# Kernel tuning notes

Measured on AMD Instinct MI355X. Metric: run time of the kernel, lower is better.

Reference implementation:

```python
import jax, jax.numpy as jnp
import numpy as np
from jax.ops import segment_sum

N_GRAPHS, N_PER = 100, 1000
N = N_GRAPHS * N_PER
DEG = 32
E = N * DEG
RATIO = 0.8
K = int(np.ceil(RATIO * N_PER))  # 800, equal-size graphs -> fixed k
F_IN, F_MID, F_OUT = 128, 16, 256


def setup_inputs() -> dict:
    key = jax.random.key(0)
    ks = jax.random.split(key, 10)
    x = jax.random.normal(ks[0], (N, F_IN), dtype=jnp.float32)
    # intra-graph random edges
    epg = E // N_GRAPHS
    src_l = jax.random.randint(ks[1], (N_GRAPHS, epg), 0, N_PER)
    dst_l = jax.random.randint(ks[2], (N_GRAPHS, epg), 0, N_PER)
    offs = (jnp.arange(N_GRAPHS) * N_PER)[:, None]
    edge_index = jnp.stack([(src_l + offs).reshape(-1), (dst_l + offs).reshape(-1)]).astype(jnp.int32)
    batch = jnp.repeat(jnp.arange(N_GRAPHS, dtype=jnp.int32), N_PER)
    s = lambda fan: 1.0 / np.sqrt(fan)
    W1 = jax.random.normal(ks[3], (F_IN, F_MID), dtype=jnp.float32) * s(F_IN)
    b1 = jnp.zeros((F_MID,), dtype=jnp.float32)
    w_rel = jax.random.normal(ks[4], (F_MID, 1), dtype=jnp.float32) * s(F_MID)
    b_rel = jnp.zeros((1,), dtype=jnp.float32)
    w_root = jax.random.normal(ks[5], (F_MID, 1), dtype=jnp.float32) * s(F_MID)
    W2 = jax.random.normal(ks[6], (F_MID, F_OUT), dtype=jnp.float32) * s(F_MID)
    b2 = jnp.zeros((F_OUT,), dtype=jnp.float32)
    return {"x": x, "edge_index": edge_index, "batch": batch,
            "W1": W1, "b1": b1, "w_rel": w_rel, "b_rel": b_rel,
            "w_root": w_root, "W2": W2, "b2": b2}


def _gcn(x, src, dst, W, b, self_w, ew, n):
    # GCNConv with self-loops: D^{-1/2}(A+I)D^{-1/2} X W + b; masked variant
    deg = segment_sum(ew, dst, num_segments=n) + self_w
    dis = jnp.where(deg > 0, jax.lax.rsqrt(deg), 0.0)
    xw = x @ W
    coef = ew * dis[src] * dis[dst]                       # [E]
    agg = segment_sum(xw[src] * coef[:, None], dst, num_segments=n)
    agg = agg + xw * (self_w * dis * dis)[:, None]        # self-loop term
    return agg + b


def reference(x, edge_index, batch, W1, b1, w_rel, b_rel, w_root, W2, b2):
    src, dst = edge_index[0], edge_index[1]
    ones_n = jnp.ones((N,), dtype=x.dtype)
    ones_e = jnp.ones((src.shape[0],), dtype=x.dtype)
    # conv1 + relu
    h = jax.nn.relu(_gcn(x, src, dst, W1, b1, ones_n, ones_e, N))
    # SAGPooling score: GraphConv(16,1) -> tanh
    agg = segment_sum(h[src], dst, num_segments=N)
    score = jnp.tanh((agg @ w_rel + h @ w_root + b_rel)[:, 0])  # [N]
    # per-graph top-k (equal graph sizes -> fixed K), expressed as node mask
    sc2 = score.reshape(N_GRAPHS, N_PER)
    _, idx = jax.lax.top_k(sc2, K)
    mask = jnp.zeros((N_GRAPHS, N_PER), dtype=x.dtype)
    mask = mask.at[jnp.arange(N_GRAPHS)[:, None], idx].set(1.0).reshape(-1)  # [N]
    h = h * (score * mask)[:, None]                       # x[perm] * score[perm]
    em = mask[src] * mask[dst]                            # filter_adj as edge mask
    # conv2 + relu on surviving nodes only
    h2 = jax.nn.relu(_gcn(h, src, dst, W2, b2, mask, em, N)) * mask[:, None]
    # global mean pool over surviving nodes per graph
    sums = segment_sum(h2, batch, num_segments=N_GRAPHS)
    cnt = segment_sum(mask, batch, num_segments=N_GRAPHS)
    return sums / cnt[:, None]
```

## Files before the change

kernel.cpp:

```cpp
#include <hip/hip_runtime.h>
#include <math.h>

#define N_NODES 100000
#define NG 100
#define N_PER 1000
#define N_EDGES 3200000
#define EPG 32000
#define EPG4 8000
#define EPGP 35008
#define K_TOP 800
#define F_IN 128
#define F_MID 16
#define F_OUT 256
#define SENT 1000
#define NCH 8
#define CHN 128

typedef __attribute__((ext_vector_type(8))) short short8;
typedef __attribute__((ext_vector_type(4))) float floatx4;

__device__ __forceinline__ unsigned short f2bf(float x) {
    union { float f; unsigned int u; } c; c.f = x;
    unsigned int u = c.u;
    u = u + 0x7FFF + ((u >> 16) & 1);
    return (unsigned short)(u >> 16);
}
__device__ __forceinline__ void add4(float4& a, const float4 b) {
    a.x += b.x; a.y += b.y; a.z += b.z; a.w += b.w;
}
__device__ __forceinline__ int fidx4(int s, int l) {
    return s * 16 + ((4 * (l + ((s >> 1) & 3))) & 15);
}
__device__ __forceinline__ unsigned int fkey(float f) {
    unsigned int u = __float_as_uint(f);
    return (u & 0x80000000u) ? ~u : (u | 0x80000000u);
}

__global__ __launch_bounds__(1024) void k_front(const float* __restrict__ x,
    const float* __restrict__ W1, const int* __restrict__ ei,
    unsigned short* __restrict__ csr, int* __restrict__ crG,
    float* __restrict__ dis1G, float* __restrict__ xw1)
{
    __shared__ int cnts[N_PER];
    __shared__ int rs[N_PER];
    __shared__ int wtot[64];
    __shared__ __align__(16) unsigned short csrl[EPGP];

    int b = blockIdx.x, t = threadIdx.x;
    if (b < NG) {
        int g = b, ebase = g * EPG, nbase = g * N_PER;
        if (b == 0 && t < F_MID) xw1[(size_t)N_NODES * F_MID + t] = 0.f;
        const int4* dst4 = (const int4*)(ei + N_EDGES + ebase);
        const int4* src4 = (const int4*)(ei + ebase);
        if (t < N_PER) cnts[t] = 0;
        __syncthreads();
        uint2 spk[8], dpk[8];
        unsigned rkreg[8];
#pragma unroll
        for (int j = 0; j < 8; j++) {
            int i = t + (j << 10);
            if (i < EPG4) {
                int4 s = src4[i];
                int4 d = dst4[i];
                unsigned dl0 = (unsigned)(d.x - nbase), dl1 = (unsigned)(d.y - nbase);
                unsigned dl2 = (unsigned)(d.z - nbase), dl3 = (unsigned)(d.w - nbase);
                spk[j].x = (unsigned)(s.x - nbase) | ((unsigned)(s.y - nbase) << 16);
                spk[j].y = (unsigned)(s.z - nbase) | ((unsigned)(s.w - nbase) << 16);
                dpk[j].x = dl0 | (dl1 << 16);
                dpk[j].y = dl2 | (dl3 << 16);
                unsigned r0 = (unsigned)atomicAdd(&cnts[dl0], 1);
                unsigned r1 = (unsigned)atomicAdd(&cnts[dl1], 1);
                unsigned r2 = (unsigned)atomicAdd(&cnts[dl2], 1);
                unsigned r3 = (unsigned)atomicAdd(&cnts[dl3], 1);
                rkreg[j] = r0 | (r1 << 8) | (r2 << 16) | (r3 << 24);
            }
        }
        __syncthreads();
        if (t < 64) {
            volatile int* vt = wtot;
            int base = t << 4;
            int lex[16]; int run = 0;
#pragma unroll
            for (int j = 0; j < 16; j++) {
                int idx = base + j;
                int c4j = (idx < N_PER) ? ((cnts[idx] + 3) & ~3) : 0;
                lex[j] = run; run += c4j;
            }
            vt[t] = run;
#pragma unroll
            for (int d = 1; d < 64; d <<= 1) {
                int v = (t >= d) ? vt[t - d] : 0;
                vt[t] = vt[t] + v;
            }
            int off = vt[t] - run;
#pragma unroll
            for (int j = 0; j < 16; j++) {
                int idx = base + j;
                if (idx < N_PER) rs[idx] = off + lex[j];
            }
        }
        __syncthreads();
        int c = (t < N_PER) ? cnts[t] : 0;
        int c4 = (c + 3) & ~3;
        if (t < N_PER) {
            int exc = rs[t];
            crG[nbase + t] = (c << 16) | exc;
            dis1G[nbase + t] = rsqrtf((float)c + 1.0f);
            for (int q = c; q < c4; q++) csrl[exc + q] = (unsigned short)SENT;
        }
        __syncthreads();
#pragma unroll
        for (int j = 0; j < 8; j++) {
            int i = t + (j << 10);
            if (i < EPG4) {
                unsigned rk = rkreg[j];
                unsigned dx = dpk[j].x, dy = dpk[j].y;
                unsigned sx = spk[j].x, sy = spk[j].y;
                csrl[rs[dx & 0xFFFFu] + (rk & 255u)]          = (unsigned short)(sx & 0xFFFFu);
                csrl[rs[dx >> 16]     + ((rk >> 8) & 255u)]   = (unsigned short)(sx >> 16);
                csrl[rs[dy & 0xFFFFu] + ((rk >> 16) & 255u)]  = (unsigned short)(sy & 0xFFFFu);
                csrl[rs[dy >> 16]     + (rk >> 24)]           = (unsigned short)(sy >> 16);
            }
        }
        __syncthreads();
        {
            const uint4* sv = (const uint4*)csrl;
            uint4* dv = (uint4*)(csr + (size_t)g * EPGP);
            for (int i = t; i < EPGP / 8; i += 1024) dv[i] = sv[i];
        }
    } else {
        int n = (b - NG) * 1024 + t;
        if (n >= N_NODES) return;
        const float4* xr = (const float4*)(x + (size_t)n * F_IN);
        float4 a0 = {0,0,0,0}, a1 = a0, a2 = a0, a3 = a0;
#pragma unroll 4
        for (int kk = 0; kk < 32; kk++) {
            float4 xv = xr[kk];
#pragma unroll
            for (int r = 0; r < 4; r++) {
                const float4* wr = (const float4*)(W1 + (kk * 4 + r) * F_MID);
                float xs = (r == 0) ? xv.x : (r == 1) ? xv.y : (r == 2) ? xv.z : xv.w;
                float4 w0 = wr[0], w1 = wr[1], w2 = wr[2], w3 = wr[3];
                a0.x = fmaf(xs, w0.x, a0.x); a0.y = fmaf(xs, w0.y, a0.y);
                a0.z = fmaf(xs, w0.z, a0.z); a0.w = fmaf(xs, w0.w, a0.w);
                a1.x = fmaf(xs, w1.x, a1.x); a1.y = fmaf(xs, w1.y, a1.y);
                a1.z = fmaf(xs, w1.z, a1.z); a1.w = fmaf(xs, w1.w, a1.w);
                a2.x = fmaf(xs, w2.x, a2.x); a2.y = fmaf(xs, w2.y, a2.y);
                a2.z = fmaf(xs, w2.z, a2.z); a2.w = fmaf(xs, w2.w, a2.w);
                a3.x = fmaf(xs, w3.x, a3.x); a3.y = fmaf(xs, w3.y, a3.y);
                a3.z = fmaf(xs, w3.z, a3.z); a3.w = fmaf(xs, w3.w, a3.w);
            }
        }
        float4* op = (float4*)(xw1 + (size_t)n * F_MID);
        op[0] = a0; op[1] = a1; op[2] = a2; op[3] = a3;
    }
}

__global__ __launch_bounds__(512) void k_conv1(const unsigned short* __restrict__ csr,
    const int* __restrict__ crG,
    const float* __restrict__ dis1G, const float* __restrict__ xw1,
    const float* __restrict__ b1, const float* __restrict__ w_rel,
    const float* __restrict__ w_root,
    float* __restrict__ hG, float* __restrict__ hwG, float* __restrict__ hroG)
{
    __shared__ __align__(16) float feat[(N_PER + 1) * F_MID];
    int t = threadIdx.x, b = blockIdx.x;
    int g = b % NG, chunk = b / NG;
    int nbase = g * N_PER;
    const unsigned short* cg = csr + (size_t)g * EPGP;
    {
        const float4* xsrc = (const float4*)(xw1 + (size_t)nbase * F_MID);
        for (int i = t; i < N_PER * 4; i += 512) {
            int nn = i >> 2, q = i & 3;
            float4 v = xsrc[i];
            float d = dis1G[nbase + nn];
            v.x *= d; v.y *= d; v.z *= d; v.w *= d;
            *(float4*)(feat + fidx4(nn, q)) = v;
        }
        if (t < 4) { float4 z = {0.f, 0.f, 0.f, 0.f}; *(float4*)(feat + fidx4(SENT, t)) = z; }
    }
    __syncthreads();

    int grp = t >> 2, l = t & 3;
    int n = chunk * CHN + grp;
    if (n >= N_PER) return;
    int cr = crG[nbase + n];
    int c4 = ((cr >> 16) + 3) & ~3;
    const unsigned short* cp = cg + (cr & 0xFFFF);
    float4 a0 = {0,0,0,0}, a1 = a0, a2 = a0, a3 = a0;
    for (int k = 0; k < c4; k += 4) {
        uint2 wv = *(const uint2*)(cp + k);
        int s0 = wv.x & 0xFFFF, s1 = wv.x >> 16, s2 = wv.y & 0xFFFF, s3 = wv.y >> 16;
        add4(a0, *(const float4*)(feat + fidx4(s0, l)));
        add4(a1, *(const float4*)(feat + fidx4(s1, l)));
        add4(a2, *(const float4*)(feat + fidx4(s2, l)));
        add4(a3, *(const float4*)(feat + fidx4(s3, l)));
    }
    add4(a0, a1); add4(a2, a3); add4(a0, a2);
    float dn = dis1G[nbase + n];
    float4 sf = *(const float4*)(feat + fidx4(n, l));
    float4 b14 = *(const float4*)(b1 + 4 * l);
    float4 hv;
    hv.x = fmaxf(fmaf(dn, a0.x + sf.x, b14.x), 0.f);
    hv.y = fmaxf(fmaf(dn, a0.y + sf.y, b14.y), 0.f);
    hv.z = fmaxf(fmaf(dn, a0.z + sf.z, b14.z), 0.f);
    hv.w = fmaxf(fmaf(dn, a0.w + sf.w, b14.w), 0.f);
    *(float4*)(hG + ((size_t)(nbase + n) << 4) + 4 * l) = hv;

    float4 wr4 = *(const float4*)(w_rel + 4 * l);
    float4 wo4 = *(const float4*)(w_root + 4 * l);
    float p1 = hv.x * wr4.x + hv.y * wr4.y + hv.z * wr4.z + hv.w * wr4.w;
    float p2 = hv.x * wo4.x + hv.y * wo4.y + hv.z * wo4.z + hv.w * wo4.w;
    p1 += __shfl_xor(p1, 1); p1 += __shfl_xor(p1, 2);
    p2 += __shfl_xor(p2, 1); p2 += __shfl_xor(p2, 2);
    if (l == 0) { hwG[nbase + n] = p1; hroG[nbase + n] = p2; }
}

__global__ __launch_bounds__(1024) void k_mid(const unsigned short* __restrict__ csr,
    const int* __restrict__ crG,
    const float* __restrict__ hwG, const float* __restrict__ hroG,
    const float* __restrict__ b_rel,
    float* __restrict__ mskG, float* __restrict__ dis2G, float* __restrict__ wsrcG,
    float* __restrict__ out)
{
    __shared__ float hwl[N_PER + 1];
    __shared__ float sc[N_PER];
    __shared__ float msk[N_PER + 1];
    __shared__ int cntl[N_PER];
    __shared__ int rsl[N_PER];
    __shared__ int hist[1024];
    __shared__ int wtot[64];
    __shared__ int sh_b1, sh_r1, sh_b2, sh_r2, sh_len, sh_cntgt, sh_T;
    __shared__ float sh_thr;

    int t = threadIdx.x, g = blockIdx.x;
    int nbase = g * N_PER;
    const unsigned short* cg = csr + (size_t)g * EPGP;
    int grp = t >> 2, l = t & 3;

    if (t < N_PER) {
        int cr = crG[nbase + t];
        cntl[t] = cr >> 16; rsl[t] = cr & 0xFFFF;
        hwl[t] = hwG[nbase + t];
    }
    if (t == 0) { sh_cntgt = 0; sh_len = 0; hwl[SENT] = 0.f; }
    if (t < F_OUT) out[g * F_OUT + t] = 0.f;
    float brel = b_rel[0];
    __syncthreads();

#pragma unroll
    for (int rr = 0; rr < 4; rr++) {
        int n = grp + 256 * rr;
        if (n < N_PER) {
            int c4 = (cntl[n] + 3) & ~3;
            const unsigned short* cp = cg + rsl[n];
            float sm = 0.f;
            for (int k = 0; k < c4; k += 4) {
                uint2 wv = *(const uint2*)(cp + k);
                int s = (l == 0) ? (int)(wv.x & 0xFFFF) : (l == 1) ? (int)(wv.x >> 16)
                      : (l == 2) ? (int)(wv.y & 0xFFFF) : (int)(wv.y >> 16);
                sm += hwl[s];
            }
            sm += __shfl_xor(sm, 1); sm += __shfl_xor(sm, 2);
            if (l == 0) sc[n] = tanhf(sm + hroG[nbase + n] + brel);
        }
    }
    __syncthreads();

    unsigned int mykey = (t < N_PER) ? fkey(sc[t]) : 0u;
    hist[t] = 0;
    __syncthreads();
    if (t < N_PER) atomicAdd(&hist[mykey >> 22], 1);
    __syncthreads();
    int hv1 = hist[t];
    __syncthreads();
    if (t < 64) {
        volatile int* vt = wtot;
        int base = t << 4;
        int vv[16]; int lex[16]; int run = 0;
#pragma unroll
        for (int j = 0; j < 16; j++) { vv[j] = hist[base + j]; lex[j] = run; run += vv[j]; }
        vt[t] = run;
#pragma unroll
        for (int d = 1; d < 64; d <<= 1) { int v = (t >= d) ? vt[t - d] : 0; vt[t] = vt[t] + v; }
        int off = vt[t] - run;
        if (t == 63) sh_T = off + run;
#pragma unroll
        for (int j = 0; j < 16; j++) hist[base + j] = off + lex[j] + vv[j];
    }
    __syncthreads();
    {
        int P = hist[t], T = sh_T;
        if (P > T - K_TOP && P - hv1 <= T - K_TOP) { sh_b1 = t; sh_r1 = K_TOP - T + P; }
    }
    __syncthreads();
    int b1v = sh_b1, r1 = sh_r1;
    hist[t] = 0;
    __syncthreads();
    if (t < N_PER && (int)(mykey >> 22) == b1v) atomicAdd(&hist[(mykey >> 12) & 1023], 1);
    __syncthreads();
    int hv2 = hist[t];
    __syncthreads();
    if (t < 64) {
        volatile int* vt = wtot;
        int base = t << 4;
        int vv[16]; int lex[16]; int run = 0;
#pragma unroll
        for (int j = 0; j < 16; j++) { vv[j] = hist[base + j]; lex[j] = run; run += vv[j]; }
        vt[t] = run;
#pragma unroll
        for (int d = 1; d < 64; d <<= 1) { int v = (t >= d) ? vt[t - d] : 0; vt[t] = vt[t] + v; }
        int off = vt[t] - run;
        if (t == 63) sh_T = off + run;
#pragma unroll
        for (int j = 0; j < 16; j++) hist[base + j] = off + lex[j] + vv[j];
    }
    __syncthreads();
    {
        int P = hist[t], T = sh_T;
        if (P > T - r1 && P - hv2 <= T - r1) { sh_b2 = t; sh_r2 = r1 - T + P; }
    }
    __syncthreads();
    unsigned int pref = ((unsigned int)b1v << 10) | (unsigned int)sh_b2;
    int r2 = sh_r2;
    __syncthreads();
    if (t < N_PER && (mykey >> 12) == pref) { int p = atomicAdd(&sh_len, 1); hist[p] = (int)mykey; }
    __syncthreads();
    {
        int L = sh_len;
        if (t < L) {
            unsigned int k0 = (unsigned int)hist[t];
            int gcnt = 0, ecnt = 0;
            for (int q2 = 0; q2 < L; q2++) {
                unsigned int kq = (unsigned int)hist[q2];
                gcnt += (kq > k0); ecnt += (kq == k0);
            }
            if (gcnt < r2 && r2 <= gcnt + ecnt)
                sh_thr = __uint_as_float((k0 & 0x80000000u) ? (k0 & 0x7FFFFFFFu) : ~k0);
        }
    }
    __syncthreads();
    float thr = sh_thr;

    {
        bool pred = (t < N_PER) && (sc[t] > thr);
        unsigned long long bal = __ballot(pred);
        if ((t & 63) == 0) atomicAdd(&sh_cntgt, (int)__popcll(bal));
    }
    __syncthreads();
    {
        int need = K_TOP - sh_cntgt;
        if (t < N_PER) {
            float v = sc[t];
            float mm;
            if (v > thr) mm = 1.f;
            else if (v < thr) mm = 0.f;
            else {
                int r = 0;
                for (int q2 = 0; q2 < t; q2++) if (sc[q2] == thr) r++;
                mm = (r < need) ? 1.f : 0.f;
            }
            msk[t] = mm;
        }
        if (t == 0) msk[SENT] = 0.f;
    }
    __syncthreads();

#pragma unroll
    for (int rr = 0; rr < 4; rr++) {
        int n = grp + 256 * rr;
        if (n < N_PER) {
            int c4 = (cntl[n] + 3) & ~3;
            const unsigned short* cp = cg + rsl[n];
            float sm = 0.f;
            for (int k = 0; k < c4; k += 4) {
                uint2 wv = *(const uint2*)(cp + k);
                int s = (l == 0) ? (int)(wv.x & 0xFFFF) : (l == 1) ? (int)(wv.x >> 16)
                      : (l == 2) ? (int)(wv.y & 0xFFFF) : (int)(wv.y >> 16);
                sm += msk[s];
            }
            sm += __shfl_xor(sm, 1); sm += __shfl_xor(sm, 2);
            if (l == 0) {
                float d2 = msk[n] * (sm + 1.f);
                float di = (d2 > 0.f) ? rsqrtf(d2) : 0.f;
                mskG[nbase + n] = msk[n];
                dis2G[nbase + n] = di;
                wsrcG[nbase + n] = sc[n] * msk[n] * di;
            }
        }
    }
}

__global__ __launch_bounds__(512) void k_conv2(const unsigned short* __restrict__ csr,
    const int* __restrict__ crG,
    const float* __restrict__ hG, const float* __restrict__ wsrcG,
    const float* __restrict__ dis2G, const float* __restrict__ mskG,
    const float* __restrict__ W2, const float* __restrict__ b2,
    float* __restrict__ out)
{
    __shared__ __align__(16) float feat2[(N_PER + 1) * F_MID];
    __shared__ __align__(16) unsigned short fbf[CHN * F_MID];
    __shared__ __align__(16) unsigned short w2t[F_OUT * F_MID];
    __shared__ float mskl[CHN];
    int t = threadIdx.x, b = blockIdx.x;
    int g = b % NG, chunk = b / NG;
    int nbase = g * N_PER, n0 = chunk * CHN;
    const unsigned short* cg = csr + (size_t)g * EPGP;

    {
        const float4* hsrc = (const float4*)(hG + (size_t)nbase * F_MID);
        for (int i = t; i < N_PER * 4; i += 512) {
            int nn = i >> 2, q = i & 3;
            float4 v = hsrc[i];
            float w = wsrcG[nbase + nn];
            v.x *= w; v.y *= w; v.z *= w; v.w *= w;
            *(float4*)(feat2 + fidx4(nn, q)) = v;
        }
        if (t < 4) { float4 z = {0.f, 0.f, 0.f, 0.f}; *(float4*)(feat2 + fidx4(SENT, t)) = z; }
    }
    for (int i = t; i < F_OUT * F_MID; i += 512) {
        int f = i >> 4, jj = i & 15;
        w2t[i] = f2bf(W2[jj * F_OUT + f]);
    }
    __syncthreads();

    int grp = t >> 2, l = t & 3;
    int n = n0 + grp;
    if (n < N_PER) {
        float di = dis2G[nbase + n];
        float4 pv = {0.f, 0.f, 0.f, 0.f};
        if (di != 0.f) {
            int cr = crG[nbase + n];
            int c4 = ((cr >> 16) + 3) & ~3;
            const unsigned short* cp = cg + (cr & 0xFFFF);
            float4 a0 = {0,0,0,0}, a1 = a0, a2 = a0, a3 = a0;
            for (int k = 0; k < c4; k += 4) {
                uint2 wv = *(const uint2*)(cp + k);
                int s0 = wv.x & 0xFFFF, s1 = wv.x >> 16, s2 = wv.y & 0xFFFF, s3 = wv.y >> 16;
                add4(a0, *(const float4*)(feat2 + fidx4(s0, l)));
                add4(a1, *(const float4*)(feat2 + fidx4(s1, l)));
                add4(a2, *(const float4*)(feat2 + fidx4(s2, l)));
                add4(a3, *(const float4*)(feat2 + fidx4(s3, l)));
            }
            add4(a0, a1); add4(a2, a3); add4(a0, a2);
            float4 sf = *(const float4*)(feat2 + fidx4(n, l));
            pv.x = di * (a0.x + sf.x);
            pv.y = di * (a0.y + sf.y);
            pv.z = di * (a0.z + sf.z);
            pv.w = di * (a0.w + sf.w);
        }
        unsigned int pk0 = (unsigned int)f2bf(pv.x) | ((unsigned int)f2bf(pv.y) << 16);
        unsigned int pk1 = (unsigned int)f2bf(pv.z) | ((unsigned int)f2bf(pv.w) << 16);
        *(unsigned int*)(fbf + grp * F_MID + 4 * l) = pk0;
        *(unsigned int*)(fbf + grp * F_MID + 4 * l + 2) = pk1;
        if (l == 0) mskl[grp] = mskG[nbase + n];
    } else {
        *(unsigned int*)(fbf + grp * F_MID + 4 * l) = 0u;
        *(unsigned int*)(fbf + grp * F_MID + 4 * l + 2) = 0u;
        if (l == 0) mskl[grp] = 0.f;
    }
    __syncthreads();

    {
        int wave = t >> 6, lane = t & 63;
        int q = lane >> 4, fl = lane & 15;
        int c0 = 32 * wave + fl, c1 = c0 + 16;
        float b2f0 = b2[c0], b2f1 = b2[c1];
        short8 bfrag0 = {0,0,0,0,0,0,0,0}, bfrag1 = bfrag0;
        if (q < 2) {
            bfrag0 = *(const short8*)(w2t + c0 * F_MID + q * 8);
            bfrag1 = *(const short8*)(w2t + c1 * F_MID + q * 8);
        }
        floatx4 zero = {0.f, 0.f, 0.f, 0.f};
        float acc0 = 0.f, acc1 = 0.f;
        for (int tile = 0; tile < CHN / 16; tile++) {
            short8 afrag = {0,0,0,0,0,0,0,0};
            int na = tile * 16 + fl;
            if (q < 2)
                afrag = *(const short8*)(fbf + na * F_MID + q * 8);
            floatx4 d0 = __builtin_amdgcn_mfma_f32_16x16x32_bf16(afrag, bfrag0, zero, 0, 0, 0);
            floatx4 d1 = __builtin_amdgcn_mfma_f32_16x16x32_bf16(afrag, bfrag1, zero, 0, 0, 0);
#pragma unroll
            for (int r = 0; r < 4; r++) {
                int nd = tile * 16 + q * 4 + r;
                float m = mskl[nd];
                acc0 += m * fmaxf(d0[r] + b2f0, 0.f);
                acc1 += m * fmaxf(d1[r] + b2f1, 0.f);
            }
        }
        acc0 += __shfl_xor(acc0, 16); acc0 += __shfl_xor(acc0, 32);
        acc1 += __shfl_xor(acc1, 16); acc1 += __shfl_xor(acc1, 32);
        if (lane < 16) {
            atomicAdd(&out[g * F_OUT + c0], acc0 * (1.0f / (float)K_TOP));
            atomicAdd(&out[g * F_OUT + c1], acc1 * (1.0f / (float)K_TOP));
        }
    }
}

extern "C" void kernel_launch(void* const* d_in, const int* in_sizes, int n_in,
                              void* d_out, int out_size, void* d_ws, size_t ws_size,
                              hipStream_t stream) {
    const float* x      = (const float*)d_in[0];
    const int*   ei     = (const int*)d_in[1];
    const float* W1     = (const float*)d_in[3];
    const float* b1     = (const float*)d_in[4];
    const float* w_rel  = (const float*)d_in[5];
    const float* b_rel  = (const float*)d_in[6];
    const float* w_root = (const float*)d_in[7];
    const float* W2     = (const float*)d_in[8];
    const float* b2     = (const float*)d_in[9];
    float* out = (float*)d_out;

    char* ws = (char*)d_ws;
    size_t o = 0;
    auto nxt = [&](size_t bytes) { void* p = ws + o; o += (bytes + 255) & ~(size_t)255; return p; };
    unsigned short* csr = (unsigned short*)nxt((size_t)NG * EPGP * sizeof(unsigned short));
    int*   crG   = (int*)nxt((size_t)N_NODES * sizeof(int));
    float* dis1G = (float*)nxt((size_t)N_NODES * sizeof(float));
    float* xw1   = (float*)nxt(((size_t)N_NODES + 1) * F_MID * sizeof(float));
    float* hG    = (float*)nxt(((size_t)N_NODES + 1) * F_MID * sizeof(float));
    float* hwG   = (float*)nxt((size_t)N_NODES * sizeof(float));
    float* hroG  = (float*)nxt((size_t)N_NODES * sizeof(float));
    float* mskG  = (float*)nxt((size_t)N_NODES * sizeof(float));
    float* dis2G = (float*)nxt((size_t)N_NODES * sizeof(float));
    float* wsrcG = (float*)nxt((size_t)N_NODES * sizeof(float));

    int gemm_blocks = (N_NODES + 1023) / 1024;
    k_front<<<NG + gemm_blocks, 1024, 0, stream>>>(x, W1, ei, csr, crG, dis1G, xw1);
    k_conv1<<<NG * NCH, 512, 0, stream>>>(csr, crG, dis1G, xw1, b1, w_rel, w_root, hG, hwG, hroG);
    k_mid<<<NG, 1024, 0, stream>>>(csr, crG, hwG, hroG, b_rel, mskG, dis2G, wsrcG, out);
    k_conv2<<<NG * NCH, 512, 0, stream>>>(csr, crG, hG, wsrcG, dis2G, mskG, W2, b2, out);
}
```

Baseline: 213.5 us.

## Stage W1 in LDS and split x@W1 rows across four lanes

The x@W1 part of the front kernel now copies W1 into shared memory with a padded stride, and gives each node to four lanes instead of one. Each lane handles an interleaved quarter of the 128 input features, and the partial sums are combined with xor shuffles. This targets the poorly coalesced per-thread row reads of x and the repeated global reads of W1, and it launches four times as many GEMM blocks. In exchange it adds a block-wide sync, an LDS fill in every block, and 16 shuffle-reductions per node, and only one lane in four writes the result.

```diff
diff --git a/kernel.cpp b/kernel.cpp
--- a/kernel.cpp
+++ b/kernel.cpp
@@ -15,6 +15,7 @@
 #define SENT 1000
 #define NCH 8
 #define CHN 128
+#define WSTRIDE 20
 
 typedef __attribute__((ext_vector_type(8))) short short8;
 typedef __attribute__((ext_vector_type(4))) float floatx4;
@@ -129,17 +130,25 @@
             for (int i = t; i < EPGP / 8; i += 1024) dv[i] = sv[i];
         }
     } else {
-        int n = (b - NG) * 1024 + t;
+        float* w1s = (float*)csrl;
+        for (int i = t; i < F_IN * F_MID; i += 1024) {
+            int row = i >> 4, col = i & 15;
+            w1s[row * WSTRIDE + col] = W1[i];
+        }
+        __syncthreads();
+        int nl = t >> 2, l = t & 3;
+        int n = (b - NG) * 256 + nl;
         if (n >= N_NODES) return;
-        const float4* xr = (const float4*)(x + (size_t)n * F_IN);
+        const float* xb = x + (size_t)n * F_IN + l * 4;
         float4 a0 = {0,0,0,0}, a1 = a0, a2 = a0, a3 = a0;
-#pragma unroll 4
-        for (int kk = 0; kk < 32; kk++) {
-            float4 xv = xr[kk];
-#pragma unroll
-            for (int r = 0; r < 4; r++) {
-                const float4* wr = (const float4*)(W1 + (kk * 4 + r) * F_MID);
-                float xs = (r == 0) ? xv.x : (r == 1) ? xv.y : (r == 2) ? xv.z : xv.w;
+#pragma unroll
+        for (int kk = 0; kk < 8; kk++) {
+            float4 xv = *(const float4*)(xb + kk * 16);
+#pragma unroll
+            for (int j = 0; j < 4; j++) {
+                int k = kk * 16 + l * 4 + j;
+                float xs = (j == 0) ? xv.x : (j == 1) ? xv.y : (j == 2) ? xv.z : xv.w;
+                const float4* wr = (const float4*)(w1s + k * WSTRIDE);
                 float4 w0 = wr[0], w1 = wr[1], w2 = wr[2], w3 = wr[3];
                 a0.x = fmaf(xs, w0.x, a0.x); a0.y = fmaf(xs, w0.y, a0.y);
                 a0.z = fmaf(xs, w0.z, a0.z); a0.w = fmaf(xs, w0.w, a0.w);
@@ -151,8 +160,16 @@
                 a3.z = fmaf(xs, w3.z, a3.z); a3.w = fmaf(xs, w3.w, a3.w);
             }
         }
-        float4* op = (float4*)(xw1 + (size_t)n * F_MID);
-        op[0] = a0; op[1] = a1; op[2] = a2; op[3] = a3;
+#define KRED(c) c += __shfl_xor(c, 1); c += __shfl_xor(c, 2);
+        KRED(a0.x) KRED(a0.y) KRED(a0.z) KRED(a0.w)
+        KRED(a1.x) KRED(a1.y) KRED(a1.z) KRED(a1.w)
+        KRED(a2.x) KRED(a2.y) KRED(a2.z) KRED(a2.w)
+        KRED(a3.x) KRED(a3.y) KRED(a3.z) KRED(a3.w)
+#undef KRED
+        if (l == 0) {
+            float4* op = (float4*)(xw1 + (size_t)n * F_MID);
+            op[0] = a0; op[1] = a1; op[2] = a2; op[3] = a3;
+        }
     }
 }
 
@@ -525,7 +542,7 @@
     float* dis2G = (float*)nxt((size_t)N_NODES * sizeof(float));
     float* wsrcG = (float*)nxt((size_t)N_NODES * sizeof(float));
 
-    int gemm_blocks = (N_NODES + 1023) / 1024;
+    int gemm_blocks = (N_NODES + 255) / 256;
     k_front<<<NG + gemm_blocks, 1024, 0, stream>>>(x, W1, ei, csr, crG, dis1G, xw1);
     k_conv1<<<NG * NCH, 512, 0, stream>>>(csr, crG, dis1G, xw1, b1, w_rel, w_root, hG, hwG, hroG);
     k_mid<<<NG, 1024, 0, stream>>>(csr, crG, hwG, hroG, b_rel, mskG, dis2G, wsrcG, out);
```

After: 196.4 us. 1.09x faster.
